# Kernel tuning notes

Measured on AMD Instinct MI355X. Metric: run time of the kernel, lower is better.

The kernel has to match this reference:

```python
import jax, jax.numpy as jnp
import numpy as np

# Band partition of the 2049 frequency bins (BSRNN-style: narrow low bands, wide high bands)
_WIDTHS = [25] * 10 + [50] * 12 + [100] * 8 + [399]
_STARTS = np.concatenate([[0], np.cumsum(_WIDTHS)])
SUBBANDS = [(int(_STARTS[i]), int(_STARTS[i + 1])) for i in range(len(_WIDTHS))]
C_IN = 2          # stereo complex input channels
OUT_CH = 128      # band embedding dim
EPS = 1e-5        # GroupNorm eps
TOTAL_CH = sum(2 * C_IN * (e - s) for s, e in SUBBANDS)  # 8196


def setup_inputs() -> dict:
    key = jax.random.key(0)
    k1, k2, k3, k4 = jax.random.split(key, 4)
    B, F, T = 8, 2049, 512
    # x is view_as_real of a complex spectrogram: [B, C, F, T, 2]
    x = jax.random.normal(k1, (B, C_IN, F, T), dtype=jnp.float32)
    x = jnp.stack([x, jax.random.normal(k2, (B, C_IN, F, T), dtype=jnp.float32)], axis=-1)
    gamma = jax.random.uniform(k3, (TOTAL_CH,), dtype=jnp.float32)            # GroupNorm weight (concat over bands)
    beta = jax.random.normal(k4, (TOTAL_CH,), dtype=jnp.float32) * 0.1       # GroupNorm bias
    W = jax.random.normal(jax.random.fold_in(key, 5), (OUT_CH, TOTAL_CH), dtype=jnp.float32) * 0.02  # 1x1 conv weights, concat over bands
    b = jax.random.normal(jax.random.fold_in(key, 6), (len(SUBBANDS), OUT_CH), dtype=jnp.float32) * 0.02
    return {"x": x, "gamma": gamma, "beta": beta, "W": W, "b": b}


def reference(x, gamma, beta, W, b):
    # x: [B, C, F, T, 2] (real view of complex spectrogram)
    B, C, F, T, _ = x.shape
    outs = []
    off = 0
    for i, (s, e) in enumerate(SUBBANDS):
        ch = 2 * C * (e - s)
        # moveaxis(-1, 1): [B, 2, C, w, T] -> reshape [B, 2*C*w, T]
        h = jnp.moveaxis(x[:, :, s:e, :, :], -1, 1).reshape(B, ch, T)
        # GroupNorm(1, ch): normalize over (channel, time) per sample
        mu = jnp.mean(h, axis=(1, 2), keepdims=True)
        var = jnp.var(h, axis=(1, 2), keepdims=True)
        g = gamma[off:off + ch][None, :, None]
        bt = beta[off:off + ch][None, :, None]
        hn = (h - mu) * jax.lax.rsqrt(var + EPS) * g + bt
        # 1x1 Conv1d == per-timestep linear: [out, ch] x [B, ch, T] -> [B, out, T]
        y = jnp.einsum('oc,bct->bot', W[:, off:off + ch], hn) + b[i][None, :, None]
        outs.append(y)
        off += ch
    return jnp.stack(outs, axis=2)  # [B, OUT_CH, n_bands, T]
```

## Files before the change

### kernel.cpp

```cpp
#include <hip/hip_runtime.h>
#include <hip/hip_bf16.h>

typedef __attribute__((ext_vector_type(8))) short short8;
typedef __attribute__((ext_vector_type(4))) float f32x4;

#define NBANDS 31
#define BB 8
#define CCH 2
#define FF 2049
#define TTS 512
#define OUTC 128
#define TCH 8196
#define EPSV 1e-5f
#define NTILES 298

__constant__ int c_wid[NBANDS] = {
    25,25,25,25,25,25,25,25,25,25,
    50,50,50,50,50,50,50,50,50,50,50,50,
    100,100,100,100,100,100,100,100,
    399};
__constant__ int c_start[NBANDS] = {
    0,25,50,75,100,125,150,175,200,225,
    250,300,350,400,450,500,550,600,650,700,750,800,
    850,950,1050,1150,1250,1350,1450,1550,
    1650};
__constant__ int c_cumf[NBANDS + 1] = {
    0,1,2,3,4,5,6,7,8,9,
    10,12,14,16,18,20,22,24,26,28,30,32,
    34,38,42,46,50,54,58,62,
    66,79};
__constant__ int c_kpad[NBANDS] = {
    128,128,128,128,128,128,128,128,128,128,
    256,256,256,256,256,256,256,256,256,256,256,256,
    448,448,448,448,448,448,448,448,
    1600};
__constant__ int c_kbase[NBANDS] = {
    0,16384,32768,49152,65536,81920,98304,114688,131072,147456,
    163840,196608,229376,262144,294912,327680,360448,393216,425984,458752,491520,524288,
    557056,614400,671744,729088,786432,843776,901120,958464,
    1015808};
__constant__ int tb16b[NBANDS] = {
    0,4,8,12,16,20,24,28,32,36,
    40,48,56,64,72,80,88,96,104,112,120,128,
    136,150,164,178,192,206,220,234,
    248};
__constant__ int c_order[NBANDS] = {
    30,22,23,24,25,26,27,28,29,
    10,11,12,13,14,15,16,17,18,19,20,21,
    0,1,2,3,4,5,6,7,8,9};

#define NSTATS 1264
#define NWPREP 248
#define NWP2   992

__device__ inline unsigned short f2bf(float f) {
    __hip_bfloat16 h = __float2bfloat16(f);
    unsigned short u;
    __builtin_memcpy(&u, &h, 2);
    return u;
}

__device__ inline void gload_lds16(const void* g, void* l) {
    __builtin_amdgcn_global_load_lds((const __attribute__((address_space(1))) void*)g,
                                     (__attribute__((address_space(3))) void*)l, 16, 0, 0);
}

__global__ __launch_bounds__(256) void prep(const float* __restrict__ x,
                                            const float* __restrict__ W,
                                            const float* __restrict__ gamma,
                                            const float* __restrict__ beta,
                                            const float* __restrict__ bias,
                                            float* __restrict__ st,
                                            float* __restrict__ wgam,
                                            float* __restrict__ wcb,
                                            unsigned short* __restrict__ wgP,
                                            unsigned short* __restrict__ xb16) {
    __shared__ float s1[256], s2[256];
    const int bid = blockIdx.x;
    const int tid = threadIdx.x;

    if (bid < NSTATS) {
        int bx  = bid >> 4;
        int ycc = bid & 15;
        int band = 0;
        while (band + 1 < NBANDS && bx >= c_cumf[band + 1]) band++;
        int fc = bx - c_cumf[band];
        int b  = ycc >> 1;
        int cc = ycc & 1;
        int w = c_wid[band], s = c_start[band];
        int nfb = (w + 15) >> 4;
        int fb0 = fc * 2;
        int nfbl = min(2, nfb - fb0);

        int lane = tid & 63, l15 = lane & 15, lg = lane >> 4;
        int tquad = tid >> 6;
        const float* xcc = x + (size_t)(b * CCH + cc) * FF * 1024;

        float sum = 0.f, sq = 0.f;
        int ntg = nfbl * 8;
        for (int tg = 0; tg < ntg; ++tg) {
            int tile = tg * 4 + tquad;
            int tb = tile & 31, fbl = tile >> 5;
            int fb = fb0 + fbl;
            int t = tb * 16 + l15;
            short8 v8;
#pragma unroll
            for (int rr = 0; rr < 4; ++rr) {
                int f = fb * 16 + 4 * lg + rr;
                float2 v = make_float2(0.f, 0.f);
                if (f < w)
                    v = *(const float2*)(xcc + (size_t)(s + f) * 1024 + t * 2);
                sum += v.x + v.y;
                sq  += v.x * v.x + v.y * v.y;
                v8[2 * rr]     = (short)f2bf(v.x);
                v8[2 * rr + 1] = (short)f2bf(v.y);
            }
            int taug = tb16b[band] + fb * 2 + cc;
            *(short8*)(xb16 + (((size_t)b * NTILES + taug) * 32 + tb) * 512 + lane * 8) = v8;
        }
        s1[tid] = sum; s2[tid] = sq;
        __syncthreads();
        for (int st_ = 128; st_ > 0; st_ >>= 1) {
            if (tid < st_) { s1[tid] += s1[tid + st_]; s2[tid] += s2[tid + st_]; }
            __syncthreads();
        }
        if (tid == 0) {
            float* dst = st + (size_t)(bx * 16 + ycc) * 2;
            dst[0] = s1[0];
            dst[1] = s2[0];
        }
    } else if (bid < NSTATS + NWPREP) {
        int r = bid - NSTATS;
        int band = r >> 3;
        int off = 4 * c_start[band];
        int ch  = 4 * c_wid[band];
        int o = (r & 7) * 16 + (tid >> 4);
        int lane = tid & 15;
        const float* wrow = W + (size_t)o * TCH + off;
        float sg = 0.f, sb = 0.f;
        for (int c = lane; c < ch; c += 16) {
            float wv = wrow[c];
            sg += wv * gamma[off + c];
            sb += wv * beta[off + c];
        }
        for (int m = 8; m; m >>= 1) {
            sg += __shfl_down(sg, m, 16);
            sb += __shfl_down(sb, m, 16);
        }
        if (lane == 0) {
            wgam[band * OUTC + o] = sg;
            wcb[band * OUTC + o]  = sb + bias[band * OUTC + o];
        }
    } else {
        int r = bid - (NSTATS + NWPREP);
        int band = r % NBANDS;
        int gy   = r / NBANDS;
        int w = c_wid[band];
        int s4 = 4 * c_start[band];
        int Kpad = c_kpad[band];
        int base = c_kbase[band];
        int N = OUTC * Kpad;
        for (int idx = gy * 256 + tid; idx < N; idx += 32 * 256) {
            int o = idx / Kpad;
            int k = idx - o * Kpad;
            int tau = k >> 5, fb = tau >> 1, cc = tau & 1;
            int fo = (k & 31) >> 1, ri = k & 1;
            int f = fb * 16 + fo;
            float val = 0.f;
            if (f < w) {
                int c = s4 + ri * 2 * w + cc * w + f;
                val = W[(size_t)o * TCH + c] * gamma[c];
            }
            int slot = (k >> 3) & 7;
            int pos = (k >> 6) * 8192 + o * 64 + ((slot ^ (o & 7)) * 8) + (k & 7);
            wgP[base + pos] = f2bf(val);
        }
    }
}

__global__ __launch_bounds__(256) void gemm_mfma(const unsigned short* __restrict__ xb16,
                                                 const unsigned short* __restrict__ wgP,
                                                 const float* __restrict__ st,
                                                 const float* __restrict__ wgam,
                                                 const float* __restrict__ wcb,
                                                 float* __restrict__ out) {
    const int band = c_order[blockIdx.y];
    const int b    = blockIdx.x >> 2;
    const int tti  = blockIdx.x & 3;
    const int tt0  = tti * 128;
    const int w    = c_wid[band];
    const int nch  = c_kpad[band] >> 6;
    const unsigned short* wgA = wgP + c_kbase[band];

    __shared__ unsigned short lA[2][8192];

    const int tid  = threadIdx.x;
    const int lane = tid & 63;
    const int wv   = tid >> 6;
    const int l15  = lane & 15;
    const int lg   = lane >> 4;

    const unsigned short* xbT = xb16 +
        (((size_t)b * NTILES + tb16b[band]) * 32 + tti * 8 + wv * 2) * 512 + lane * 8;

    f32x4 acc[8][2] = {};
    short8 bA[4], bB[4];

#define LOADB(c, dst) do {                                                     \
    _Pragma("unroll")                                                          \
    for (int kk = 0; kk < 2; ++kk)                                             \
        _Pragma("unroll")                                                      \
        for (int nf = 0; nf < 2; ++nf)                                         \
            dst[kk * 2 + nf] =                                                 \
                *(const short8*)(xbT + (size_t)((2 * (c) + kk) * 32 + nf) * 512); \
} while (0)

#define STAGE(c, buf) do {                                                     \
    const unsigned short* srcc = wgA + (size_t)(c) * 8192;                     \
    _Pragma("unroll")                                                          \
    for (int q = 0; q < 4; ++q)                                                \
        gload_lds16(srcc + q * 2048 + tid * 8, &lA[buf][q * 2048 + tid * 8]);  \
} while (0)

#define COMPUTE(br, buf) do {                                                  \
    _Pragma("unroll")                                                          \
    for (int kk = 0; kk < 2; ++kk) {                                           \
        short8 af[8];                                                          \
        _Pragma("unroll")                                                      \
        for (int m = 0; m < 8; ++m) {                                          \
            int o = m * 16 + l15;                                              \
            int slot = (lg + 4 * kk) ^ (o & 7);                                \
            af[m] = *(const short8*)&lA[buf][o * 64 + slot * 8];               \
        }                                                                      \
        _Pragma("unroll")                                                      \
        for (int nf = 0; nf < 2; ++nf)                                         \
            _Pragma("unroll")                                                  \
            for (int m = 0; m < 8; ++m)                                        \
                acc[m][nf] = __builtin_amdgcn_mfma_f32_16x16x32_bf16(          \
                    af[m], br[kk * 2 + nf], acc[m][nf], 0, 0, 0);              \
    }                                                                          \
} while (0)

    LOADB(0, bA);
    STAGE(0, 0);
    __syncthreads();
    for (int c = 0; c < nch; c += 2) {
        if (c + 1 < nch) { LOADB(c + 1, bB); STAGE(c + 1, 1); }
        COMPUTE(bA, 0);
        __syncthreads();
        if (c + 1 < nch) {
            if (c + 2 < nch) { LOADB(c + 2, bA); STAGE(c + 2, 0); }
            COMPUTE(bB, 1);
            __syncthreads();
        }
    }
#undef LOADB
#undef STAGE
#undef COMPUTE

    float sum = 0.f, sq = 0.f;
    {
        int cc0 = c_cumf[band], cc1 = c_cumf[band + 1];
        for (int c = cc0; c < cc1; ++c) {
            const float* p0 = st + (size_t)(c * 16 + b * 2) * 2;
            sum += p0[0] + p0[2];
            sq  += p0[1] + p0[3];
        }
    }
    const float Nf = (float)(w * 2048);
    const float mu = sum / Nf;
    const float rs = rsqrtf(sq / Nf - mu * mu + EPSV);

#pragma unroll
    for (int m = 0; m < 8; ++m) {
#pragma unroll
        for (int r = 0; r < 4; ++r) {
            int o = m * 16 + lg * 4 + r;
            float wg = wgam[band * OUTC + o];
            float cb = wcb[band * OUTC + o];
            size_t rowoff = (((size_t)b * OUTC + o) * NBANDS + band) * TTS;
#pragma unroll
            for (int nf = 0; nf < 2; ++nf) {
                int t = tt0 + wv * 32 + nf * 16 + l15;
                out[rowoff + t] = rs * (acc[m][nf][r] - mu * wg) + cb;
            }
        }
    }
}

extern "C" void kernel_launch(void* const* d_in, const int* in_sizes, int n_in,
                              void* d_out, int out_size, void* d_ws, size_t ws_size,
                              hipStream_t stream) {
    const float* x     = (const float*)d_in[0];
    const float* gamma = (const float*)d_in[1];
    const float* beta  = (const float*)d_in[2];
    const float* W     = (const float*)d_in[3];
    const float* bias  = (const float*)d_in[4];
    float* out = (float*)d_out;
    float* ws  = (float*)d_ws;

    float* st_part = ws;
    float* wgam    = ws + 3072;
    float* wcb     = ws + 7168;
    unsigned short* wgP  = (unsigned short*)(ws + 11264);
    unsigned short* xb16 = (unsigned short*)(ws + 622592);

    prep<<<NSTATS + NWPREP + NWP2, 256, 0, stream>>>(x, W, gamma, beta, bias,
                                                     st_part, wgam, wcb, wgP, xb16);
    gemm_mfma<<<dim3(32, NBANDS), 256, 0, stream>>>(xb16, wgP, st_part, wgam, wcb, out);
}
```

Before: 98.09 us.

## Stage input rows through LDS with async global-to-LDS loads in transpose prep

```diff
diff --git a/kernel.cpp b/kernel.cpp
--- a/kernel.cpp
+++ b/kernel.cpp
@@ -24,11 +24,11 @@
     250,300,350,400,450,500,550,600,650,700,750,800,
     850,950,1050,1150,1250,1350,1450,1550,
     1650};
-__constant__ int c_cumf[NBANDS + 1] = {
-    0,1,2,3,4,5,6,7,8,9,
-    10,12,14,16,18,20,22,24,26,28,30,32,
-    34,38,42,46,50,54,58,62,
-    66,79};
+__constant__ int c_gb0[NBANDS + 1] = {
+    0,2,4,6,8,10,12,14,16,18,
+    20,24,28,32,36,40,44,48,52,56,60,64,
+    68,75,82,89,96,103,110,117,
+    124,149};
 __constant__ int c_kpad[NBANDS] = {
     128,128,128,128,128,128,128,128,128,128,
     256,256,256,256,256,256,256,256,256,256,256,256,
@@ -49,7 +49,7 @@
     10,11,12,13,14,15,16,17,18,19,20,21,
     0,1,2,3,4,5,6,7,8,9};
 
-#define NSTATS 1264
+#define NTRANS 2384
 #define NWPREP 248
 #define NWP2   992
 
@@ -75,49 +75,54 @@
                                             float* __restrict__ wcb,
                                             unsigned short* __restrict__ wgP,
                                             unsigned short* __restrict__ xb16) {
+    __shared__ __align__(16) float ltf[16384];
     __shared__ float s1[256], s2[256];
     const int bid = blockIdx.x;
     const int tid = threadIdx.x;
 
-    if (bid < NSTATS) {
-        int bx  = bid >> 4;
+    if (bid < NTRANS) {
+        int g   = bid >> 4;
         int ycc = bid & 15;
         int band = 0;
-        while (band + 1 < NBANDS && bx >= c_cumf[band + 1]) band++;
-        int fc = bx - c_cumf[band];
+        while (band + 1 < NBANDS && g >= c_gb0[band + 1]) band++;
+        int fb = g - c_gb0[band];
         int b  = ycc >> 1;
         int cc = ycc & 1;
         int w = c_wid[band], s = c_start[band];
-        int nfb = (w + 15) >> 4;
-        int fb0 = fc * 2;
-        int nfbl = min(2, nfb - fb0);
-
-        int lane = tid & 63, l15 = lane & 15, lg = lane >> 4;
-        int tquad = tid >> 6;
+        int f0 = fb * 16;
         const float* xcc = x + (size_t)(b * CCH + cc) * FF * 1024;
 
+#pragma unroll
+        for (int r = 0; r < 16; ++r) {
+            int row = s + min(f0 + r, w - 1);
+            gload_lds16(xcc + (size_t)row * 1024 + tid * 4, &ltf[r * 1024 + tid * 4]);
+        }
+        __syncthreads();
+
+        int taug = tb16b[band] + fb * 2 + cc;
+        unsigned short* dst = xb16 + ((size_t)b * NTILES + taug) * 16384;
         float sum = 0.f, sq = 0.f;
-        int ntg = nfbl * 8;
-        for (int tg = 0; tg < ntg; ++tg) {
-            int tile = tg * 4 + tquad;
-            int tb = tile & 31, fbl = tile >> 5;
-            int fb = fb0 + fbl;
+#pragma unroll
+        for (int it = 0; it < 8; ++it) {
+            int idx = it * 256 + tid;
+            int tb = idx >> 6, lane = idx & 63;
+            int l15 = lane & 15, lg = lane >> 4;
             int t = tb * 16 + l15;
-            short8 v8;
+            short8 w8;
 #pragma unroll
             for (int rr = 0; rr < 4; ++rr) {
-                int f = fb * 16 + 4 * lg + rr;
-                float2 v = make_float2(0.f, 0.f);
-                if (f < w)
-                    v = *(const float2*)(xcc + (size_t)(s + f) * 1024 + t * 2);
+                int floc = 4 * lg + rr;
+                float2 v = *(const float2*)&ltf[floc * 1024 + t * 2];
+                if (f0 + floc >= w) v = make_float2(0.f, 0.f);
                 sum += v.x + v.y;
                 sq  += v.x * v.x + v.y * v.y;
-                v8[2 * rr]     = (short)f2bf(v.x);
-                v8[2 * rr + 1] = (short)f2bf(v.y);
+                w8[2 * rr]     = (short)f2bf(v.x);
+                w8[2 * rr + 1] = (short)f2bf(v.y);
             }
-            int taug = tb16b[band] + fb * 2 + cc;
-            *(short8*)(xb16 + (((size_t)b * NTILES + taug) * 32 + tb) * 512 + lane * 8) = v8;
-        }
+            *(short8*)(dst + (size_t)idx * 8) = w8;
+        }
+
+        __syncthreads();
         s1[tid] = sum; s2[tid] = sq;
         __syncthreads();
         for (int st_ = 128; st_ > 0; st_ >>= 1) {
@@ -125,12 +130,12 @@
             __syncthreads();
         }
         if (tid == 0) {
-            float* dst = st + (size_t)(bx * 16 + ycc) * 2;
-            dst[0] = s1[0];
-            dst[1] = s2[0];
-        }
-    } else if (bid < NSTATS + NWPREP) {
-        int r = bid - NSTATS;
+            float* dp = st + (size_t)(g * 16 + ycc) * 2;
+            dp[0] = s1[0];
+            dp[1] = s2[0];
+        }
+    } else if (bid < NTRANS + NWPREP) {
+        int r = bid - NTRANS;
         int band = r >> 3;
         int off = 4 * c_start[band];
         int ch  = 4 * c_wid[band];
@@ -152,7 +157,7 @@
             wcb[band * OUTC + o]  = sb + bias[band * OUTC + o];
         }
     } else {
-        int r = bid - (NSTATS + NWPREP);
+        int r = bid - (NTRANS + NWPREP);
         int band = r % NBANDS;
         int gy   = r / NBANDS;
         int w = c_wid[band];
@@ -260,9 +265,9 @@
 
     float sum = 0.f, sq = 0.f;
     {
-        int cc0 = c_cumf[band], cc1 = c_cumf[band + 1];
-        for (int c = cc0; c < cc1; ++c) {
-            const float* p0 = st + (size_t)(c * 16 + b * 2) * 2;
+        int g0 = c_gb0[band], g1 = c_gb0[band + 1];
+        for (int g = g0; g < g1; ++g) {
+            const float* p0 = st + (size_t)(g * 16 + b * 2) * 2;
             sum += p0[0] + p0[2];
             sq  += p0[1] + p0[3];
         }
@@ -300,12 +305,12 @@
     float* ws  = (float*)d_ws;
 
     float* st_part = ws;
-    float* wgam    = ws + 3072;
-    float* wcb     = ws + 7168;
-    unsigned short* wgP  = (unsigned short*)(ws + 11264);
-    unsigned short* xb16 = (unsigned short*)(ws + 622592);
-
-    prep<<<NSTATS + NWPREP + NWP2, 256, 0, stream>>>(x, W, gamma, beta, bias,
+    float* wgam    = ws + 5120;
+    float* wcb     = ws + 9216;
+    unsigned short* wgP  = (unsigned short*)(ws + 13312);
+    unsigned short* xb16 = (unsigned short*)(ws + 640000);
+
+    prep<<<NTRANS + NWPREP + NWP2, 256, 0, stream>>>(x, W, gamma, beta, bias,
                                                      st_part, wgam, wcb, wgP, xb16);
     gemm_mfma<<<dim3(32, NBANDS), 256, 0, stream>>>(xb16, wgP, st_part, wgam, wcb, out);
 }
```

Result: slower. 105.5 us (+7.6%).
